# Performance work log

Hardware: AMD Instinct MI355X
Metric: run time of the kernel (lower is better)

Reference implementation:

```python
import jax, jax.numpy as jnp
import numpy as np

EPS = 1e-8

def setup_inputs() -> dict:
    key = jax.random.key(0)
    k1, k2 = jax.random.split(key)
    x1 = jax.random.normal(k1, (16, 4096, 256), dtype=jnp.float32)
    x2 = jax.random.normal(k2, (16, 4096, 256), dtype=jnp.float32)
    return {"x1": x1, "x2": x2}

def _l2_normalize(x):
    # matches F.normalize / torch norm-with-clamp: x / max(||x||, eps)
    n = jnp.linalg.norm(x, axis=-1, keepdims=True)
    return x / jnp.maximum(n, EPS)

def reference(x1, x2):
    # cosine distance: mean over all segment pairs of (1 - cos_sim)
    # mean_{i,j} (1 - x1n_i . x2n_j) == 1 - (mean_i x1n_i) . (mean_j x2n_j)
    # -- algebraically identical to the original per-batch mm + mean,
    # but avoids materializing the O(n_seg^2) similarity matrix.
    n_batch, embedding_dim = x1.shape[0], x1.shape[-1]
    x1 = x1.reshape(n_batch, -1, embedding_dim)
    x2 = x2.reshape(n_batch, -1, embedding_dim)
    x1n = _l2_normalize(x1)  # (B, S, D)
    x2n = _l2_normalize(x2)
    m1 = x1n.mean(axis=1)    # (B, D)
    m2 = x2n.mean(axis=1)    # (B, D)
    return 1.0 - jnp.einsum('bd,bd->b', m1, m2)  # (B,)
```

## Files before the change

kernel.cpp:

```cpp
#include <hip/hip_runtime.h>


constexpr int D = 256;
constexpr int S = 4096;
constexpr int B = 16;
constexpr int BLOCKS_PER_PAIR = 64;
constexpr int WAVES_PER_BLOCK = 4;
constexpr int WAVES_PER_PAIR  = BLOCKS_PER_PAIR * WAVES_PER_BLOCK;
constexpr int ROWS_PER_WAVE   = S / WAVES_PER_PAIR;
constexpr int NPAIR = 2 * B;
constexpr int NBLK1 = NPAIR * BLOCKS_PER_PAIR;
constexpr float EPS2 = 1e-16f;

template <bool USE_PARTIALS>
__global__ __launch_bounds__(256) void row_norm_sum_kernel(
    const float* __restrict__ x1, const float* __restrict__ x2,
    float* __restrict__ sums )
{
    const int pair = blockIdx.x / BLOCKS_PER_PAIR;
    const int blk  = blockIdx.x % BLOCKS_PER_PAIR;
    const int w    = threadIdx.x >> 6;
    const int lane = threadIdx.x & 63;
    const int sub  = lane & 15;
    const int g    = lane >> 4;
    const int wv   = blk * WAVES_PER_BLOCK + w;

    const int batch = pair >> 1;
    const float* __restrict__ src = (pair & 1) ? x2 : x1;
    src += (size_t)batch * S * D;

    const float* __restrict__ lbase =
        src + (size_t)(wv * ROWS_PER_WAVE + g) * D + sub * 4;

    float4 a0 = make_float4(0.f,0.f,0.f,0.f);
    float4 a1 = a0, a2 = a0, a3 = a0;
    float4 va0, va1, va2, va3, vb0, vb1, vb2, vb3;

#define LOADV(v0,v1,v2,v3, i)  do {                     \
    const float* p_ = lbase + (size_t)(i) * 4 * D;      \
    v0 = *(const float4*)(p_ +   0);                    \
    v1 = *(const float4*)(p_ +  64);                    \
    v2 = *(const float4*)(p_ + 128);                    \
    v3 = *(const float4*)(p_ + 192); } while (0)

#define STEPV(v0,v1,v2,v3) do {                                        \
    float ss = v0.x*v0.x + v0.y*v0.y + v0.z*v0.z + v0.w*v0.w           \
             + v1.x*v1.x + v1.y*v1.y + v1.z*v1.z + v1.w*v1.w           \
             + v2.x*v2.x + v2.y*v2.y + v2.z*v2.z + v2.w*v2.w           \
             + v3.x*v3.x + v3.y*v3.y + v3.z*v3.z + v3.w*v3.w;          \
    ss += __shfl_xor(ss, 1, 64);                                       \
    ss += __shfl_xor(ss, 2, 64);                                       \
    ss += __shfl_xor(ss, 4, 64);                                       \
    ss += __shfl_xor(ss, 8, 64);                                       \
    const float sc_ = rsqrtf(fmaxf(ss, EPS2));                         \
    a0.x += v0.x*sc_; a0.y += v0.y*sc_; a0.z += v0.z*sc_; a0.w += v0.w*sc_; \
    a1.x += v1.x*sc_; a1.y += v1.y*sc_; a1.z += v1.z*sc_; a1.w += v1.w*sc_; \
    a2.x += v2.x*sc_; a2.y += v2.y*sc_; a2.z += v2.z*sc_; a2.w += v2.w*sc_; \
    a3.x += v3.x*sc_; a3.y += v3.y*sc_; a3.z += v3.z*sc_; a3.w += v3.w*sc_; \
  } while (0)

    LOADV(va0,va1,va2,va3, 0);
    LOADV(vb0,vb1,vb2,vb3, 1);
    STEPV(va0,va1,va2,va3);
    LOADV(va0,va1,va2,va3, 2);
    STEPV(vb0,vb1,vb2,vb3);
    LOADV(vb0,vb1,vb2,vb3, 3);
    STEPV(va0,va1,va2,va3);
    STEPV(vb0,vb1,vb2,vb3);

#undef LOADV
#undef STEPV

#define GRED(m_)                                                        \
    a0.x += __shfl_xor(a0.x, m_, 64); a0.y += __shfl_xor(a0.y, m_, 64); \
    a0.z += __shfl_xor(a0.z, m_, 64); a0.w += __shfl_xor(a0.w, m_, 64); \
    a1.x += __shfl_xor(a1.x, m_, 64); a1.y += __shfl_xor(a1.y, m_, 64); \
    a1.z += __shfl_xor(a1.z, m_, 64); a1.w += __shfl_xor(a1.w, m_, 64); \
    a2.x += __shfl_xor(a2.x, m_, 64); a2.y += __shfl_xor(a2.y, m_, 64); \
    a2.z += __shfl_xor(a2.z, m_, 64); a2.w += __shfl_xor(a2.w, m_, 64); \
    a3.x += __shfl_xor(a3.x, m_, 64); a3.y += __shfl_xor(a3.y, m_, 64); \
    a3.z += __shfl_xor(a3.z, m_, 64); a3.w += __shfl_xor(a3.w, m_, 64);
    GRED(16)
    GRED(32)
#undef GRED

    __shared__ float lds[WAVES_PER_BLOCK][D];
    if (g == 0) {
        *(float4*)&lds[w][4 * sub      ] = a0;
        *(float4*)&lds[w][4 * sub +  64] = a1;
        *(float4*)&lds[w][4 * sub + 128] = a2;
        *(float4*)&lds[w][4 * sub + 192] = a3;
    }
    __syncthreads();

    const int t = threadIdx.x;
    const float val = lds[0][t] + lds[1][t] + lds[2][t] + lds[3][t];
    if (USE_PARTIALS) {
        sums[(size_t)blockIdx.x * D + t] = val;
    } else {
        atomicAdd(&sums[(size_t)pair * D + t], val);
    }
}

__global__ __launch_bounds__(256) void finalize_partials_kernel(
    const float* __restrict__ partials, float* __restrict__ out)
{
    const int b = blockIdx.x;
    const int t = threadIdx.x;
    const int w = t >> 6, lane = t & 63;

    const float* p1 = partials + ((size_t)(2 * b + 0) * BLOCKS_PER_PAIR) * D + t;
    const float* p2 = partials + ((size_t)(2 * b + 1) * BLOCKS_PER_PAIR) * D + t;
    float s1 = 0.f, s2 = 0.f;
    #pragma unroll 8
    for (int k = 0; k < BLOCKS_PER_PAIR; ++k) {
        s1 += p1[(size_t)k * D];
        s2 += p2[(size_t)k * D];
    }
    float d = s1 * s2;
    #pragma unroll
    for (int m = 1; m < 64; m <<= 1) d += __shfl_xor(d, m, 64);

    __shared__ float r[WAVES_PER_BLOCK];
    if (lane == 0) r[w] = d;
    __syncthreads();
    if (t == 0) {
        const float inv = 1.0f / ((float)S * (float)S);
        out[b] = 1.0f - (r[0] + r[1] + r[2] + r[3]) * inv;
    }
}

__global__ __launch_bounds__(64) void finalize_kernel(
    const float* __restrict__ sums, float* __restrict__ out)
{
    const int b = blockIdx.x;
    const int lane = threadIdx.x;
    const float4 a = *(const float4*)(sums + (size_t)(2 * b + 0) * D + lane * 4);
    const float4 c = *(const float4*)(sums + (size_t)(2 * b + 1) * D + lane * 4);
    float d = a.x * c.x + a.y * c.y + a.z * c.z + a.w * c.w;
    #pragma unroll
    for (int m = 1; m < 64; m <<= 1) d += __shfl_xor(d, m, 64);
    if (lane == 0) {
        const float inv = 1.0f / ((float)S * (float)S);
        out[b] = 1.0f - d * inv;
    }
}

extern "C" void kernel_launch(void* const* d_in, const int* in_sizes, int n_in,
                              void* d_out, int out_size, void* d_ws, size_t ws_size,
                              hipStream_t stream) {
    const float* x1 = (const float*)d_in[0];
    const float* x2 = (const float*)d_in[1];
    float* out = (float*)d_out;
    float* ws = (float*)d_ws;

    const size_t partial_bytes = (size_t)NBLK1 * D * sizeof(float);
    if (ws_size >= partial_bytes) {
        row_norm_sum_kernel<true><<<NBLK1, 256, 0, stream>>>(x1, x2, ws);
        finalize_partials_kernel<<<B, 256, 0, stream>>>(ws, out);
    } else {
        hipMemsetAsync(ws, 0, (size_t)NPAIR * D * sizeof(float), stream);
        row_norm_sum_kernel<false><<<NBLK1, 256, 0, stream>>>(x1, x2, ws);
        finalize_kernel<<<B, 64, 0, stream>>>(ws, out);
    }
}
```

Measured before the change: 148.7 us.

## Fuse finalize into main kernel via last-block counter; use DPP row reductions

Merges the separate finalize kernel into the row-norm kernel. Each block writes its partial, bumps a per-batch global counter, and the last block of each batch reduces all partials and writes the output, which removes one kernel launch. It also replaces the 16-lane shuffle reduction with DPP row operations, and replaces the cross-group shuffle reduction with LDS stores into a padded array. The cost is extra thread fences and an atomic per block, and the counter relies on modulo wraparound across calls.

```diff
diff --git a/kernel.cpp b/kernel.cpp
--- a/kernel.cpp
+++ b/kernel.cpp
@@ -10,12 +10,30 @@
 constexpr int ROWS_PER_WAVE   = S / WAVES_PER_PAIR;
 constexpr int NPAIR = 2 * B;
 constexpr int NBLK1 = NPAIR * BLOCKS_PER_PAIR;
+constexpr int BLOCKS_PER_BATCH = 2 * BLOCKS_PER_PAIR;
 constexpr float EPS2 = 1e-16f;
 
-template <bool USE_PARTIALS>
-__global__ __launch_bounds__(256) void row_norm_sum_kernel(
+__device__ unsigned g_ctrs[B];
+
+template <int CTRL>
+__device__ __forceinline__ float dpp_add(float x) {
+    int y = __builtin_amdgcn_update_dpp(0, __float_as_int(x), CTRL, 0xF, 0xF, true);
+    return x + __int_as_float(y);
+}
+__device__ __forceinline__ float row16_allsum(float ss) {
+    ss = dpp_add<0xB1>(ss);
+    ss = dpp_add<0x4E>(ss);
+    ss = dpp_add<0x141>(ss);
+    ss = dpp_add<0x140>(ss);
+    return ss;
+}
+
+template <int MODE>
+__global__ __launch_bounds__(256, 8) void embdist_kernel(
     const float* __restrict__ x1, const float* __restrict__ x2,
-    float* __restrict__ sums )
+    float* __restrict__ partials ,
+    float* __restrict__ sums     ,
+    float* __restrict__ out      )
 {
     const int pair = blockIdx.x / BLOCKS_PER_PAIR;
     const int blk  = blockIdx.x % BLOCKS_PER_PAIR;
@@ -25,14 +43,12 @@
     const int g    = lane >> 4;
     const int wv   = blk * WAVES_PER_BLOCK + w;
 
-    const int batch = pair >> 1;
     const float* __restrict__ src = (pair & 1) ? x2 : x1;
-    src += (size_t)batch * S * D;
-
+    src += (size_t)(pair >> 1) * S * D;
     const float* __restrict__ lbase =
         src + (size_t)(wv * ROWS_PER_WAVE + g) * D + sub * 4;
 
-    float4 a0 = make_float4(0.f,0.f,0.f,0.f);
+    float4 a0 = make_float4(0.f, 0.f, 0.f, 0.f);
     float4 a1 = a0, a2 = a0, a3 = a0;
     float4 va0, va1, va2, va3, vb0, vb1, vb2, vb3;
 
@@ -48,10 +64,7 @@
              + v1.x*v1.x + v1.y*v1.y + v1.z*v1.z + v1.w*v1.w           \
              + v2.x*v2.x + v2.y*v2.y + v2.z*v2.z + v2.w*v2.w           \
              + v3.x*v3.x + v3.y*v3.y + v3.z*v3.z + v3.w*v3.w;          \
-    ss += __shfl_xor(ss, 1, 64);                                       \
-    ss += __shfl_xor(ss, 2, 64);                                       \
-    ss += __shfl_xor(ss, 4, 64);                                       \
-    ss += __shfl_xor(ss, 8, 64);                                       \
+    ss = row16_allsum(ss);                                             \
     const float sc_ = rsqrtf(fmaxf(ss, EPS2));                         \
     a0.x += v0.x*sc_; a0.y += v0.y*sc_; a0.z += v0.z*sc_; a0.w += v0.w*sc_; \
     a1.x += v1.x*sc_; a1.y += v1.y*sc_; a1.z += v1.z*sc_; a1.w += v1.w*sc_; \
@@ -71,62 +84,54 @@
 #undef LOADV
 #undef STEPV
 
-#define GRED(m_)                                                        \
-    a0.x += __shfl_xor(a0.x, m_, 64); a0.y += __shfl_xor(a0.y, m_, 64); \
-    a0.z += __shfl_xor(a0.z, m_, 64); a0.w += __shfl_xor(a0.w, m_, 64); \
-    a1.x += __shfl_xor(a1.x, m_, 64); a1.y += __shfl_xor(a1.y, m_, 64); \
-    a1.z += __shfl_xor(a1.z, m_, 64); a1.w += __shfl_xor(a1.w, m_, 64); \
-    a2.x += __shfl_xor(a2.x, m_, 64); a2.y += __shfl_xor(a2.y, m_, 64); \
-    a2.z += __shfl_xor(a2.z, m_, 64); a2.w += __shfl_xor(a2.w, m_, 64); \
-    a3.x += __shfl_xor(a3.x, m_, 64); a3.y += __shfl_xor(a3.y, m_, 64); \
-    a3.z += __shfl_xor(a3.z, m_, 64); a3.w += __shfl_xor(a3.w, m_, 64);
-    GRED(16)
-    GRED(32)
-#undef GRED
-
-    __shared__ float lds[WAVES_PER_BLOCK][D];
-    if (g == 0) {
-        *(float4*)&lds[w][4 * sub      ] = a0;
-        *(float4*)&lds[w][4 * sub +  64] = a1;
-        *(float4*)&lds[w][4 * sub + 128] = a2;
-        *(float4*)&lds[w][4 * sub + 192] = a3;
-    }
+    __shared__ float lds[WAVES_PER_BLOCK][4][260];
+    *(float4*)&lds[w][g][4 * sub      ] = a0;
+    *(float4*)&lds[w][g][4 * sub +  64] = a1;
+    *(float4*)&lds[w][g][4 * sub + 128] = a2;
+    *(float4*)&lds[w][g][4 * sub + 192] = a3;
     __syncthreads();
 
     const int t = threadIdx.x;
-    const float val = lds[0][t] + lds[1][t] + lds[2][t] + lds[3][t];
-    if (USE_PARTIALS) {
-        sums[(size_t)blockIdx.x * D + t] = val;
-    } else {
+    float val = 0.f;
+    #pragma unroll
+    for (int ww = 0; ww < WAVES_PER_BLOCK; ++ww)
+        #pragma unroll
+        for (int gg = 0; gg < 4; ++gg)
+            val += lds[ww][gg][t];
+
+    if (MODE == 1) {
         atomicAdd(&sums[(size_t)pair * D + t], val);
+        return;
     }
-}
 
-__global__ __launch_bounds__(256) void finalize_partials_kernel(
-    const float* __restrict__ partials, float* __restrict__ out)
-{
-    const int b = blockIdx.x;
-    const int t = threadIdx.x;
-    const int w = t >> 6, lane = t & 63;
+    partials[(size_t)blockIdx.x * D + t] = val;
+    __threadfence();
+    __syncthreads();
+    __shared__ unsigned old_s;
+    const int b = pair >> 1;
+    if (t == 0) old_s = atomicAdd(&g_ctrs[b], 1u);
+    __syncthreads();
 
-    const float* p1 = partials + ((size_t)(2 * b + 0) * BLOCKS_PER_PAIR) * D + t;
-    const float* p2 = partials + ((size_t)(2 * b + 1) * BLOCKS_PER_PAIR) * D + t;
-    float s1 = 0.f, s2 = 0.f;
-    #pragma unroll 8
-    for (int k = 0; k < BLOCKS_PER_PAIR; ++k) {
-        s1 += p1[(size_t)k * D];
-        s2 += p2[(size_t)k * D];
-    }
-    float d = s1 * s2;
-    #pragma unroll
-    for (int m = 1; m < 64; m <<= 1) d += __shfl_xor(d, m, 64);
-
-    __shared__ float r[WAVES_PER_BLOCK];
-    if (lane == 0) r[w] = d;
-    __syncthreads();
-    if (t == 0) {
-        const float inv = 1.0f / ((float)S * (float)S);
-        out[b] = 1.0f - (r[0] + r[1] + r[2] + r[3]) * inv;
+    if ((old_s & (BLOCKS_PER_BATCH - 1)) == (BLOCKS_PER_BATCH - 1)) {
+        __threadfence();
+        const float* p1 = partials + (size_t)(2 * b) * BLOCKS_PER_PAIR * D + t;
+        const float* p2 = p1 + (size_t)BLOCKS_PER_PAIR * D;
+        float s1 = 0.f, s2 = 0.f;
+        #pragma unroll 8
+        for (int k = 0; k < BLOCKS_PER_PAIR; ++k) {
+            s1 += p1[(size_t)k * D];
+            s2 += p2[(size_t)k * D];
+        }
+        float dsum = s1 * s2;
+        #pragma unroll
+        for (int m = 1; m < 64; m <<= 1) dsum += __shfl_xor(dsum, m, 64);
+        __shared__ float r[WAVES_PER_BLOCK];
+        if (lane == 0) r[w] = dsum;
+        __syncthreads();
+        if (t == 0) {
+            const float inv = 1.0f / ((float)S * (float)S);
+            out[b] = 1.0f - (r[0] + r[1] + r[2] + r[3]) * inv;
+        }
     }
 }
 
@@ -156,11 +161,10 @@
 
     const size_t partial_bytes = (size_t)NBLK1 * D * sizeof(float);
     if (ws_size >= partial_bytes) {
-        row_norm_sum_kernel<true><<<NBLK1, 256, 0, stream>>>(x1, x2, ws);
-        finalize_partials_kernel<<<B, 256, 0, stream>>>(ws, out);
+        embdist_kernel<0><<<NBLK1, 256, 0, stream>>>(x1, x2, ws, nullptr, out);
     } else {
         hipMemsetAsync(ws, 0, (size_t)NPAIR * D * sizeof(float), stream);
-        row_norm_sum_kernel<false><<<NBLK1, 256, 0, stream>>>(x1, x2, ws);
+        embdist_kernel<1><<<NBLK1, 256, 0, stream>>>(x1, x2, nullptr, ws, out);
         finalize_kernel<<<B, 64, 0, stream>>>(ws, out);
     }
 }
```

Result: slower. 494.2 us (+232.3%).

## Issue all loads upfront, use DPP row reductions, and reduce lane groups via LDS

Applied to the files above, without the earlier changes.

All 16 float4 loads per lane are issued before any compute, replacing the two-stage double buffer, so more memory requests are in flight at once. The 16-lane row sum of squares now uses DPP row operations instead of shfl_xor (ds_bpermute). The 32 cross-group shuffles on the accumulators are removed: every lane group writes its partial to padded LDS and each thread sums 16 entries. This trades higher register pressure and extra LDS traffic for fewer cross-lane instructions in a kernel that is mostly bound by memory bandwidth.

```diff
diff --git a/kernel.cpp b/kernel.cpp
--- a/kernel.cpp
+++ b/kernel.cpp
@@ -12,6 +12,19 @@
 constexpr int NBLK1 = NPAIR * BLOCKS_PER_PAIR;
 constexpr float EPS2 = 1e-16f;
 
+template <int CTRL>
+__device__ __forceinline__ float dpp_add(float x) {
+    int y = __builtin_amdgcn_update_dpp(0, __float_as_int(x), CTRL, 0xF, 0xF, true);
+    return x + __int_as_float(y);
+}
+__device__ __forceinline__ float row16_allsum(float ss) {
+    ss = dpp_add<0xB1>(ss);
+    ss = dpp_add<0x4E>(ss);
+    ss = dpp_add<0x141>(ss);
+    ss = dpp_add<0x140>(ss);
+    return ss;
+}
+
 template <bool USE_PARTIALS>
 __global__ __launch_bounds__(256) void row_norm_sum_kernel(
     const float* __restrict__ x1, const float* __restrict__ x2,
@@ -25,76 +38,67 @@
     const int g    = lane >> 4;
     const int wv   = blk * WAVES_PER_BLOCK + w;
 
-    const int batch = pair >> 1;
     const float* __restrict__ src = (pair & 1) ? x2 : x1;
-    src += (size_t)batch * S * D;
-
+    src += (size_t)(pair >> 1) * S * D;
     const float* __restrict__ lbase =
         src + (size_t)(wv * ROWS_PER_WAVE + g) * D + sub * 4;
 
-    float4 a0 = make_float4(0.f,0.f,0.f,0.f);
-    float4 a1 = a0, a2 = a0, a3 = a0;
-    float4 va0, va1, va2, va3, vb0, vb1, vb2, vb3;
+    float4 vv[4][4];
+    #pragma unroll
+    for (int i = 0; i < 4; ++i) {
+        const float* p_ = lbase + (size_t)i * 4 * D;
+        vv[i][0] = *(const float4*)(p_ +   0);
+        vv[i][1] = *(const float4*)(p_ +  64);
+        vv[i][2] = *(const float4*)(p_ + 128);
+        vv[i][3] = *(const float4*)(p_ + 192);
+    }
 
-#define LOADV(v0,v1,v2,v3, i)  do {                     \
-    const float* p_ = lbase + (size_t)(i) * 4 * D;      \
-    v0 = *(const float4*)(p_ +   0);                    \
-    v1 = *(const float4*)(p_ +  64);                    \
-    v2 = *(const float4*)(p_ + 128);                    \
-    v3 = *(const float4*)(p_ + 192); } while (0)
+    float ss[4];
+    #pragma unroll
+    for (int i = 0; i < 4; ++i) {
+        float s = 0.f;
+        #pragma unroll
+        for (int j = 0; j < 4; ++j)
+            s += vv[i][j].x * vv[i][j].x + vv[i][j].y * vv[i][j].y
+               + vv[i][j].z * vv[i][j].z + vv[i][j].w * vv[i][j].w;
+        ss[i] = s;
+    }
+    #pragma unroll
+    for (int i = 0; i < 4; ++i) ss[i] = row16_allsum(ss[i]);
 
-#define STEPV(v0,v1,v2,v3) do {                                        \
-    float ss = v0.x*v0.x + v0.y*v0.y + v0.z*v0.z + v0.w*v0.w           \
-             + v1.x*v1.x + v1.y*v1.y + v1.z*v1.z + v1.w*v1.w           \
-             + v2.x*v2.x + v2.y*v2.y + v2.z*v2.z + v2.w*v2.w           \
-             + v3.x*v3.x + v3.y*v3.y + v3.z*v3.z + v3.w*v3.w;          \
-    ss += __shfl_xor(ss, 1, 64);                                       \
-    ss += __shfl_xor(ss, 2, 64);                                       \
-    ss += __shfl_xor(ss, 4, 64);                                       \
-    ss += __shfl_xor(ss, 8, 64);                                       \
-    const float sc_ = rsqrtf(fmaxf(ss, EPS2));                         \
-    a0.x += v0.x*sc_; a0.y += v0.y*sc_; a0.z += v0.z*sc_; a0.w += v0.w*sc_; \
-    a1.x += v1.x*sc_; a1.y += v1.y*sc_; a1.z += v1.z*sc_; a1.w += v1.w*sc_; \
-    a2.x += v2.x*sc_; a2.y += v2.y*sc_; a2.z += v2.z*sc_; a2.w += v2.w*sc_; \
-    a3.x += v3.x*sc_; a3.y += v3.y*sc_; a3.z += v3.z*sc_; a3.w += v3.w*sc_; \
-  } while (0)
+    float sc[4];
+    #pragma unroll
+    for (int i = 0; i < 4; ++i) sc[i] = rsqrtf(fmaxf(ss[i], EPS2));
 
-    LOADV(va0,va1,va2,va3, 0);
-    LOADV(vb0,vb1,vb2,vb3, 1);
-    STEPV(va0,va1,va2,va3);
-    LOADV(va0,va1,va2,va3, 2);
-    STEPV(vb0,vb1,vb2,vb3);
-    LOADV(vb0,vb1,vb2,vb3, 3);
-    STEPV(va0,va1,va2,va3);
-    STEPV(vb0,vb1,vb2,vb3);
+    float4 acc[4];
+    #pragma unroll
+    for (int j = 0; j < 4; ++j) acc[j] = make_float4(0.f, 0.f, 0.f, 0.f);
+    #pragma unroll
+    for (int i = 0; i < 4; ++i) {
+        #pragma unroll
+        for (int j = 0; j < 4; ++j) {
+            acc[j].x += vv[i][j].x * sc[i];
+            acc[j].y += vv[i][j].y * sc[i];
+            acc[j].z += vv[i][j].z * sc[i];
+            acc[j].w += vv[i][j].w * sc[i];
+        }
+    }
 
-#undef LOADV
-#undef STEPV
-
-#define GRED(m_)                                                        \
-    a0.x += __shfl_xor(a0.x, m_, 64); a0.y += __shfl_xor(a0.y, m_, 64); \
-    a0.z += __shfl_xor(a0.z, m_, 64); a0.w += __shfl_xor(a0.w, m_, 64); \
-    a1.x += __shfl_xor(a1.x, m_, 64); a1.y += __shfl_xor(a1.y, m_, 64); \
-    a1.z += __shfl_xor(a1.z, m_, 64); a1.w += __shfl_xor(a1.w, m_, 64); \
-    a2.x += __shfl_xor(a2.x, m_, 64); a2.y += __shfl_xor(a2.y, m_, 64); \
-    a2.z += __shfl_xor(a2.z, m_, 64); a2.w += __shfl_xor(a2.w, m_, 64); \
-    a3.x += __shfl_xor(a3.x, m_, 64); a3.y += __shfl_xor(a3.y, m_, 64); \
-    a3.z += __shfl_xor(a3.z, m_, 64); a3.w += __shfl_xor(a3.w, m_, 64);
-    GRED(16)
-    GRED(32)
-#undef GRED
-
-    __shared__ float lds[WAVES_PER_BLOCK][D];
-    if (g == 0) {
-        *(float4*)&lds[w][4 * sub      ] = a0;
-        *(float4*)&lds[w][4 * sub +  64] = a1;
-        *(float4*)&lds[w][4 * sub + 128] = a2;
-        *(float4*)&lds[w][4 * sub + 192] = a3;
-    }
+    __shared__ float lds[WAVES_PER_BLOCK][4][260];
+    *(float4*)&lds[w][g][4 * sub      ] = acc[0];
+    *(float4*)&lds[w][g][4 * sub +  64] = acc[1];
+    *(float4*)&lds[w][g][4 * sub + 128] = acc[2];
+    *(float4*)&lds[w][g][4 * sub + 192] = acc[3];
     __syncthreads();
 
     const int t = threadIdx.x;
-    const float val = lds[0][t] + lds[1][t] + lds[2][t] + lds[3][t];
+    float val = 0.f;
+    #pragma unroll
+    for (int ww = 0; ww < WAVES_PER_BLOCK; ++ww)
+        #pragma unroll
+        for (int gg = 0; gg < 4; ++gg)
+            val += lds[ww][gg][t];
+
     if (USE_PARTIALS) {
         sums[(size_t)blockIdx.x * D + t] = val;
     } else {
```

After: 144.0 us. -3.2%, faster.
